# Performance work log

Hardware: AMD Instinct MI355X
Metric: run time of the kernel (lower is better)

## Reference

```python
import jax, jax.numpy as jnp
import numpy as np

V, L, D, DEMO, HID, N = 20000, 128, 256, 70, 1024, 2048


def setup_inputs() -> dict:
    key = jax.random.key(0)
    ks = jax.random.split(key, 16)
    s = 1.0 / np.sqrt(D)
    inp = {
        # learned parameters
        "E": jax.random.normal(ks[0], (V, D), jnp.float32) * 0.02,
        "Wq": jax.random.normal(ks[1], (D, D), jnp.float32) * s,
        "Wk": jax.random.normal(ks[2], (D, D), jnp.float32) * s,
        "Wv": jax.random.normal(ks[3], (D, D), jnp.float32) * s,
        "c_attn": jnp.ones((1,), jnp.float32) * 0.1,   # time_weight_net coefficient (attention decay)
        "c_pool": jnp.ones((1,), jnp.float32) * 0.5,   # history_repr Q_base-style pooling decay
        "W1": jax.random.normal(ks[4], (D + DEMO, HID), jnp.float32) * (1.0 / np.sqrt(D + DEMO)),
        "b1": jnp.zeros((HID,), jnp.float32),
        "W2": jax.random.normal(ks[5], (HID, 1), jnp.float32) * (1.0 / np.sqrt(HID)),
        "b2": jnp.zeros((1,), jnp.float32),
        # batched ragged task instances
        "demo": jax.random.normal(ks[6], (N, DEMO), jnp.float32),
        "hist_times": jax.random.uniform(ks[7], (N, L), jnp.float32) * 10.0,
        "event_time": jax.random.uniform(ks[8], (N,), jnp.float32) * 10.0 + 10.0,
        "labels": jax.random.randint(ks[9], (N,), 0, 2).astype(jnp.float32),
        "codes": jax.random.randint(ks[10], (N, L), 0, V),
        "lengths": jax.random.randint(ks[11], (N,), 1, L + 1).astype(jnp.int32),
    }
    return inp


def reference(E, Wq, Wk, Wv, c_attn, c_pool, W1, b1, W2, b2,
              demo, hist_times, event_time, labels, codes, lengths):
    POS_WEIGHT = 2.0
    NEG = jnp.float32(-1e9)
    mask = jnp.arange(L)[None, :] < lengths[:, None]            # [N, L] valid history positions

    emb = E[codes]                                              # [N, L, D] gather
    q = jnp.einsum('nld,de->nle', emb, Wq)
    k = jnp.einsum('nld,de->nle', emb, Wk)
    v = jnp.einsum('nld,de->nle', emb, Wv)

    # time-aware self-attention over each ragged history (masked)
    scores = jnp.einsum('nid,njd->nij', q, k) / jnp.sqrt(jnp.float32(D))
    dt = jnp.abs(hist_times[:, :, None] - hist_times[:, None, :])  # [N, L, L]
    scores = scores - c_attn[0] * dt
    scores = jnp.where(mask[:, None, :], scores, NEG)
    attn = jax.nn.softmax(scores, axis=-1)
    events = jnp.einsum('nij,njd->nid', attn, v)                # [N, L, D]

    # history_repr: time-decayed pooling toward event_time
    w = -c_pool[0] * (event_time[:, None] - hist_times)         # [N, L]
    w = jnp.where(mask, w, NEG)
    w = jax.nn.softmax(w, axis=-1)
    repr_ = jnp.einsum('nl,nld->nd', w, events)                 # [N, D]

    # disease/death classifier: demographics + history repr -> logit
    x = jnp.concatenate([demo, repr_], axis=-1)                 # [N, DEMO+D]
    h = jax.nn.relu(x @ W1 + b1)
    logit = (h @ W2 + b2)[:, 0]                                 # [N]

    # BCEWithLogitsLoss with pos_weight, averaged over valid predictions
    loss = -(POS_WEIGHT * labels * jax.nn.log_sigmoid(logit)
             + (1.0 - labels) * jax.nn.log_sigmoid(-logit))
    avg_loss = jnp.mean(loss)

    reg_loss = jnp.sum(c_attn ** 2) + jnp.sum(c_pool ** 2)      # time_weight_net.get_reg_loss()
    return avg_loss + reg_loss
```

## Files before the change

kernel.cpp:

```cpp
#include <hip/hip_runtime.h>
#include <hip/hip_bf16.h>
#include <math.h>
#include <stdint.h>

#define VV 20000
#define LL 128
#define DD 256
#define DEMO_ 70
#define HID_ 1024
#define NN 2048

typedef __attribute__((ext_vector_type(8))) short short8;
typedef __attribute__((ext_vector_type(4))) float f32x4;

__device__ __forceinline__ float bf2f(uint32_t u) {
    union { uint32_t u; float f; } c; c.u = u << 16; return c.f;
}
__device__ __forceinline__ uint32_t f2bf(float f) {
    union { float f; uint32_t u; } c; c.f = f;
    return (c.u + 0x7fffu + ((c.u >> 16) & 1u)) >> 16;
}

__device__ __forceinline__ int sw_off(int row, int col) {
    return (row << 8) + ((((col >> 3) ^ (row & 7)) << 3) | (col & 7));
}

__global__ __launch_bounds__(256) void k_init(const float* ca, const float* cp,
                                              float* z, float* out) {
    int idx = blockIdx.x * 256 + threadIdx.x;
    z[idx] = 0.f;
    if (idx == 0) out[0] = ca[0] * ca[0] + cp[0] * cp[0];
}

__global__ __launch_bounds__(256) void k_M(const float* __restrict__ Wq,
                                           const float* __restrict__ Wk,
                                           unsigned short* __restrict__ Mxf) {
    __shared__ float wq_s[DD];
    int e = blockIdx.x, t = threadIdx.x;
    wq_s[t] = Wq[(size_t)e * DD + t];
    __syncthreads();
    const float4* wk4 = (const float4*)(Wk + (size_t)t * DD);
    const float4* wq4 = (const float4*)wq_s;
    float4 acc = make_float4(0.f, 0.f, 0.f, 0.f);
    for (int c = 0; c < DD / 4; ++c) {
        float4 a = wq4[c]; float4 b = wk4[c];
        acc.x += a.x * b.x; acc.y += a.y * b.y;
        acc.z += a.z * b.z; acc.w += a.w * b.w;
    }
    float val = acc.x + acc.y + acc.z + acc.w;
    int frag = (e >> 4) * 8 + (t >> 5);
    int pos  = (((t >> 3) & 3) * 16 + (e & 15)) * 8 + (t & 7);
    Mxf[(size_t)frag * 512 + pos] = (unsigned short)f2bf(val);
}

__global__ __launch_bounds__(256) void k_prep(const float* __restrict__ Wv,
                                              const float* __restrict__ W1,
                                              unsigned short* __restrict__ W1f) {
    __shared__ float wv_s[DD];
    int k = blockIdx.x, t = threadIdx.x;
    int h = t + 256 * blockIdx.y;
    float val;
    if (k >= 326) {
        val = 0.f;
    } else if (k < DEMO_) {
        val = W1[(size_t)k * HID_ + h];
    } else {
        int e = k - DEMO_;
        wv_s[t] = Wv[(size_t)e * DD + t];
        __syncthreads();
        float acc = 0.f;
        for (int n = 0; n < DD; ++n)
            acc += wv_s[n] * W1[(size_t)(DEMO_ + n) * HID_ + h];
        val = acc;
    }
    int frag = (h >> 4) * 11 + (k >> 5);
    int pos  = (((k >> 3) & 3) * 16 + (h & 15)) * 8 + (k & 7);
    W1f[(size_t)frag * 512 + pos] = (unsigned short)f2bf(val);
}

__global__ __launch_bounds__(512, 4) void k_main(
    const float* __restrict__ E,
    const float* __restrict__ ht,  const float* __restrict__ evt_t,
    const int* __restrict__ codes, const int* __restrict__ lens,
    const float* __restrict__ ca_p, const float* __restrict__ cp_p,
    const unsigned short* __restrict__ Mxf,
    unsigned short* __restrict__ Rbf)
{
    __shared__ __align__(16) unsigned short emb_u[LL * DD];
    __shared__ float times_s[LL];
    __shared__ int   codes_s[LL];
    __shared__ float w_s[LL];
    __shared__ float apart[8][LL];
    __shared__ float rp_part[8][DD];
    __shared__ float asum[LL];

    const int n = blockIdx.x;
    const int tid = threadIdx.x, wv = tid >> 6, ln = tid & 63;
    const int q = ln >> 4, m = ln & 15;
    const int len = lens[n];
    const int it_n = (len + 15) >> 4;
    const float ca = ca_p[0], cp = cp_p[0];
    const float evt = evt_t[n];

    ((float*)apart)[tid]          = 0.f;
    ((float*)apart)[tid + 512]    = 0.f;
    ((float*)rp_part)[tid]        = 0.f;
    ((float*)rp_part)[tid + 512]  = 0.f;
    ((float*)rp_part)[tid + 1024] = 0.f;
    ((float*)rp_part)[tid + 1536] = 0.f;
    if (tid < LL) {
        w_s[tid] = 0.f;
        if (tid < len) {
            times_s[tid] = ht[(size_t)n * LL + tid];
            codes_s[tid] = codes[(size_t)n * LL + tid];
        }
    }
    __syncthreads();

    if (wv == 0) {
        float u0 = (ln      < len) ? cp * (times_s[ln]      - evt) : 0.f;
        float u1 = (ln + 64 < len) ? cp * (times_s[ln + 64] - evt) : 0.f;
        float e0 = (ln      < len) ? __expf(u0) : 0.f;
        float e1 = (ln + 64 < len) ? __expf(u1) : 0.f;
        float sm = e0 + e1;
        for (int o = 32; o; o >>= 1) sm += __shfl_xor(sm, o, 64);
        float inv = 1.f / sm;
        if (ln      < len) w_s[ln]      = e0 * inv;
        if (ln + 64 < len) w_s[ln + 64] = e1 * inv;
    }

    for (int l0 = wv; l0 < len; l0 += 32) {
        float4 v[4];
        #pragma unroll
        for (int u = 0; u < 4; ++u) {
            int l = l0 + u * 8;
            if (l < len)
                v[u] = ((const float4*)(E + (size_t)codes_s[l] * DD))[ln];
        }
        #pragma unroll
        for (int u = 0; u < 4; ++u) {
            int l = l0 + u * 8;
            if (l < len)
                *(uint2*)&emb_u[sw_off(l, 4 * ln)] =
                    make_uint2(f2bf(v[u].x) | (f2bf(v[u].y) << 16),
                               f2bf(v[u].z) | (f2bf(v[u].w) << 16));
        }
    }
    __syncthreads();

    short8 bB[2][8];
    #pragma unroll
    for (int nt = 0; nt < 2; ++nt)
        #pragma unroll
        for (int kk = 0; kk < 8; ++kk)
            bB[nt][kk] = *(const short8*)(Mxf + (size_t)((wv * 2 + nt) * 8 + kk) * 512 + ln * 8);

    short8 aC[8];
    for (int it = 0; it < it_n; ++it) {
        f32x4 h0 = (f32x4)0.f, h1 = (f32x4)0.f;
        #pragma unroll
        for (int kk = 0; kk < 8; ++kk) {
            short8 af = *(const short8*)&emb_u[sw_off(it * 16 + m, kk * 32 + q * 8)];
            if (it == wv) aC[kk] = af;
            h0 = __builtin_amdgcn_mfma_f32_16x16x32_bf16(af, bB[0][kk], h0, 0, 0, 0);
            h1 = __builtin_amdgcn_mfma_f32_16x16x32_bf16(af, bB[1][kk], h1, 0, 0, 0);
        }
        __syncthreads();
        #pragma unroll
        for (int r = 0; r < 4; ++r) {
            int row = it * 16 + q * 4 + r;
            emb_u[sw_off(row, wv * 32 + m)]      = (unsigned short)f2bf(h0[r]);
            emb_u[sw_off(row, wv * 32 + 16 + m)] = (unsigned short)f2bf(h1[r]);
        }
    }
    __syncthreads();

    if (wv < it_n) {
        f32x4 sac[8];
        #pragma unroll
        for (int jt = 0; jt < 8; ++jt) sac[jt] = (f32x4)0.f;
        for (int jt = 0; jt < it_n; ++jt) {
            #pragma unroll
            for (int kk = 0; kk < 8; ++kk) {
                short8 bH = *(const short8*)&emb_u[sw_off(jt * 16 + m, kk * 32 + q * 8)];
                sac[jt] = __builtin_amdgcn_mfma_f32_16x16x32_bf16(aC[kk], bH, sac[jt], 0, 0, 0);
            }
        }
        int i_base = wv * 16 + q * 4;
        float ti[4]; bool vR[4]; float rowsum[4];
        #pragma unroll
        for (int r = 0; r < 4; ++r) {
            vR[r] = (i_base + r) < len;
            ti[r] = times_s[i_base + r];
            rowsum[r] = 0.f;
        }
        for (int jt = 0; jt < it_n; ++jt) {
            int jcol = jt * 16 + m;
            bool vC = jcol < len;
            float tj = times_s[jcol];
            #pragma unroll
            for (int r = 0; r < 4; ++r) {
                float arg = sac[jt][r] * 0.0625f - ca * fabsf(ti[r] - tj);
                float p = (vR[r] && vC) ? __expf(arg) : 0.f;
                sac[jt][r] = p;
                rowsum[r] += p;
            }
        }
        #pragma unroll
        for (int r = 0; r < 4; ++r) {
            float s = rowsum[r];
            s += __shfl_xor(s, 1, 64); s += __shfl_xor(s, 2, 64);
            s += __shfl_xor(s, 4, 64); s += __shfl_xor(s, 8, 64);
            rowsum[r] = s;
        }
        float sc[4];
        #pragma unroll
        for (int r = 0; r < 4; ++r)
            sc[r] = (vR[r] && rowsum[r] > 0.f) ? w_s[i_base + r] / rowsum[r] : 0.f;
        for (int jt = 0; jt < it_n; ++jt) {
            float v = sc[0] * sac[jt][0] + sc[1] * sac[jt][1]
                    + sc[2] * sac[jt][2] + sc[3] * sac[jt][3];
            v += __shfl_xor(v, 16, 64);
            v += __shfl_xor(v, 32, 64);
            if (q == 0) apart[wv][jt * 16 + m] = v;
        }
    }
    __syncthreads();

    if (tid < LL)
        asum[tid] = apart[0][tid] + apart[1][tid] + apart[2][tid] + apart[3][tid]
                  + apart[4][tid] + apart[5][tid] + apart[6][tid] + apart[7][tid];
    __syncthreads();

    if (wv < it_n) {
        float aw = asum[wv * 16 + m];
        #pragma unroll
        for (int kk = 0; kk < 8; ++kk) {
            float v[8];
            #pragma unroll
            for (int j = 0; j < 8; ++j)
                v[j] = aw * bf2f((uint32_t)(unsigned short)aC[kk][j]);
            #pragma unroll
            for (int o = 1; o <= 8; o <<= 1)
                #pragma unroll
                for (int j = 0; j < 8; ++j)
                    v[j] += __shfl_xor(v[j], o, 64);
            if (m < 8)
                rp_part[wv][kk * 32 + q * 8 + m] = v[m];
        }
    }
    __syncthreads();
    if (tid < DD) {
        float r = rp_part[0][tid] + rp_part[1][tid] + rp_part[2][tid] + rp_part[3][tid]
                + rp_part[4][tid] + rp_part[5][tid] + rp_part[6][tid] + rp_part[7][tid];
        Rbf[(size_t)n * DD + tid] = (unsigned short)f2bf(r);
    }
}

__global__ __launch_bounds__(256) void k_mlp(
    const float* __restrict__ demo,
    const float* __restrict__ b1,   const float* __restrict__ W2,
    const unsigned short* __restrict__ Rbf,
    const unsigned short* __restrict__ W1f,
    float* __restrict__ z)
{
    __shared__ __align__(16) unsigned short xs[16][360];
    __shared__ float W2s[256];
    __shared__ float b1s[256];
    __shared__ float wred[4][16];

    const int tid = threadIdx.x, wv = tid >> 6, ln = tid & 63;
    const int q = ln >> 4, m = ln & 15;
    const int s0 = blockIdx.x * 16;
    const int by = blockIdx.y;
    const int hbase = by * 256;

    W2s[tid] = W2[hbase + tid];
    b1s[tid] = b1[hbase + tid];
    for (int s = 0; s < 16; ++s) {
        if (tid < DEMO_) xs[s][tid] = (unsigned short)f2bf(demo[(size_t)(s0 + s) * DEMO_ + tid]);
        xs[s][DEMO_ + tid] = Rbf[(size_t)(s0 + s) * DD + tid];
        if (tid < 34) xs[s][326 + tid] = 0;
    }
    __syncthreads();

    f32x4 cacc[4];
    #pragma unroll
    for (int ntl = 0; ntl < 4; ++ntl) cacc[ntl] = (f32x4)0.f;

    for (int kk = 0; kk < 11; ++kk) {
        short8 af = *(const short8*)&xs[m][kk * 32 + q * 8];
        #pragma unroll
        for (int ntl = 0; ntl < 4; ++ntl) {
            int frag = (by * 16 + wv * 4 + ntl) * 11 + kk;
            short8 bfd = *(const short8*)(W1f + (size_t)frag * 512 + ln * 8);
            cacc[ntl] = __builtin_amdgcn_mfma_f32_16x16x32_bf16(af, bfd, cacc[ntl], 0, 0, 0);
        }
    }

    float ls0 = 0.f, ls1 = 0.f, ls2 = 0.f, ls3 = 0.f;
    #pragma unroll
    for (int ntl = 0; ntl < 4; ++ntl) {
        int hl = wv * 64 + ntl * 16 + m;
        float bb = b1s[hl], w2v = W2s[hl];
        ls0 += fmaxf(cacc[ntl][0] + bb, 0.f) * w2v;
        ls1 += fmaxf(cacc[ntl][1] + bb, 0.f) * w2v;
        ls2 += fmaxf(cacc[ntl][2] + bb, 0.f) * w2v;
        ls3 += fmaxf(cacc[ntl][3] + bb, 0.f) * w2v;
    }
    #pragma unroll
    for (int o = 1; o <= 8; o <<= 1) {
        ls0 += __shfl_xor(ls0, o, 64); ls1 += __shfl_xor(ls1, o, 64);
        ls2 += __shfl_xor(ls2, o, 64); ls3 += __shfl_xor(ls3, o, 64);
    }
    if (m == 0) {
        wred[wv][q * 4 + 0] = ls0; wred[wv][q * 4 + 1] = ls1;
        wred[wv][q * 4 + 2] = ls2; wred[wv][q * 4 + 3] = ls3;
    }
    __syncthreads();
    if (tid < 16)
        atomicAdd(&z[s0 + tid], wred[0][tid] + wred[1][tid] + wred[2][tid] + wred[3][tid]);
}

__global__ __launch_bounds__(256) void k_loss(const float* __restrict__ labels,
                                              const float* __restrict__ b2,
                                              const float* __restrict__ z,
                                              float* __restrict__ out) {
    __shared__ float red[4];
    int tid = threadIdx.x, wv = tid >> 6;
    int i = blockIdx.x * 256 + tid;
    float zz = z[i] + b2[0];
    float y = labels[i];
    float lg = log1pf(__expf(-fabsf(zz)));
    float loss = 2.f * y * (fmaxf(-zz, 0.f) + lg) + (1.f - y) * (fmaxf(zz, 0.f) + lg);
    for (int o = 32; o; o >>= 1) loss += __shfl_xor(loss, o, 64);
    if ((tid & 63) == 0) red[wv] = loss;
    __syncthreads();
    if (tid == 0)
        atomicAdd(out, (red[0] + red[1] + red[2] + red[3]) * (1.f / (float)NN));
}

extern "C" void kernel_launch(void* const* d_in, const int* in_sizes, int n_in,
                              void* d_out, int out_size, void* d_ws, size_t ws_size,
                              hipStream_t stream) {
    const float* E      = (const float*)d_in[0];
    const float* Wq     = (const float*)d_in[1];
    const float* Wk     = (const float*)d_in[2];
    const float* Wv     = (const float*)d_in[3];
    const float* ca     = (const float*)d_in[4];
    const float* cp     = (const float*)d_in[5];
    const float* W1     = (const float*)d_in[6];
    const float* b1     = (const float*)d_in[7];
    const float* W2     = (const float*)d_in[8];
    const float* b2     = (const float*)d_in[9];
    const float* demo   = (const float*)d_in[10];
    const float* ht     = (const float*)d_in[11];
    const float* evt    = (const float*)d_in[12];
    const float* labels = (const float*)d_in[13];
    const int*   codes  = (const int*)d_in[14];
    const int*   lens   = (const int*)d_in[15];
    float* out = (float*)d_out;

    unsigned short* Mxf = (unsigned short*)d_ws;
    unsigned short* W1f = (unsigned short*)((char*)d_ws + 131072);
    unsigned short* Rbf = (unsigned short*)((char*)d_ws + 851968);
    float*          zar = (float*)((char*)d_ws + 1900544);

    hipLaunchKernelGGL(k_init, dim3(NN / 256), dim3(256), 0, stream, ca, cp, zar, out);
    hipLaunchKernelGGL(k_M,    dim3(DD), dim3(DD), 0, stream, Wq, Wk, Mxf);
    hipLaunchKernelGGL(k_prep, dim3(352, 4), dim3(256), 0, stream, Wv, W1, W1f);
    hipLaunchKernelGGL(k_main, dim3(NN), dim3(512), 0, stream,
                       E, ht, evt, codes, lens, ca, cp, Mxf, Rbf);
    hipLaunchKernelGGL(k_mlp,  dim3(NN / 16, 4), dim3(256), 0, stream,
                       demo, b1, W2, Rbf, W1f, zar);
    hipLaunchKernelGGL(k_loss, dim3(NN / 256), dim3(256), 0, stream, labels, b2, zar, out);
}
```

Measured before the change: 263.8 us.

## Merge prep kernels and schedule attention blocks longest-first by history length

Folds the init, Wq·Wk product and Wv·W1 prep kernels into one launch, which adds a block that counting-sorts instances by tile count so the main kernel processes longest histories first (LPT-style load balancing). The main kernel moves the Mxf fragment loads earlier to overlap with gathers and drops zero-initialisation of partial buffers. Reductions now sum only the active tiles. This cuts launch overhead and tail imbalance from ragged lengths, at the cost of an extra indirection and a serial sort block inside the prep launch.

```diff
diff --git a/kernel.cpp b/kernel.cpp
--- a/kernel.cpp
+++ b/kernel.cpp
@@ -25,57 +25,75 @@
     return (row << 8) + ((((col >> 3) ^ (row & 7)) << 3) | (col & 7));
 }
 
-__global__ __launch_bounds__(256) void k_init(const float* ca, const float* cp,
-                                              float* z, float* out) {
-    int idx = blockIdx.x * 256 + threadIdx.x;
-    z[idx] = 0.f;
-    if (idx == 0) out[0] = ca[0] * ca[0] + cp[0] * cp[0];
-}
-
-__global__ __launch_bounds__(256) void k_M(const float* __restrict__ Wq,
-                                           const float* __restrict__ Wk,
-                                           unsigned short* __restrict__ Mxf) {
-    __shared__ float wq_s[DD];
-    int e = blockIdx.x, t = threadIdx.x;
-    wq_s[t] = Wq[(size_t)e * DD + t];
-    __syncthreads();
-    const float4* wk4 = (const float4*)(Wk + (size_t)t * DD);
-    const float4* wq4 = (const float4*)wq_s;
-    float4 acc = make_float4(0.f, 0.f, 0.f, 0.f);
-    for (int c = 0; c < DD / 4; ++c) {
-        float4 a = wq4[c]; float4 b = wk4[c];
-        acc.x += a.x * b.x; acc.y += a.y * b.y;
-        acc.z += a.z * b.z; acc.w += a.w * b.w;
-    }
-    float val = acc.x + acc.y + acc.z + acc.w;
-    int frag = (e >> 4) * 8 + (t >> 5);
-    int pos  = (((t >> 3) & 3) * 16 + (e & 15)) * 8 + (t & 7);
-    Mxf[(size_t)frag * 512 + pos] = (unsigned short)f2bf(val);
-}
-
-__global__ __launch_bounds__(256) void k_prep(const float* __restrict__ Wv,
-                                              const float* __restrict__ W1,
-                                              unsigned short* __restrict__ W1f) {
-    __shared__ float wv_s[DD];
-    int k = blockIdx.x, t = threadIdx.x;
-    int h = t + 256 * blockIdx.y;
-    float val;
-    if (k >= 326) {
-        val = 0.f;
-    } else if (k < DEMO_) {
-        val = W1[(size_t)k * HID_ + h];
+__global__ __launch_bounds__(256) void k_pre(
+    const float* __restrict__ Wq, const float* __restrict__ Wk,
+    const float* __restrict__ Wv, const float* __restrict__ W1,
+    const float* __restrict__ ca, const float* __restrict__ cp,
+    const int* __restrict__ lens,
+    unsigned short* __restrict__ Mxf, unsigned short* __restrict__ W1f,
+    int* __restrict__ order, float* __restrict__ z, float* __restrict__ out)
+{
+    __shared__ float sm[DD];
+    __shared__ int cnt[9], off[9], cur[9];
+    const int b = blockIdx.x, t = threadIdx.x;
+
+    if (b < 256) {
+        int e = b;
+        sm[t] = Wq[(size_t)e * DD + t];
+        __syncthreads();
+        const float4* wk4 = (const float4*)(Wk + (size_t)t * DD);
+        const float4* wq4 = (const float4*)sm;
+        float4 acc = make_float4(0.f, 0.f, 0.f, 0.f);
+        for (int c = 0; c < DD / 4; ++c) {
+            float4 a = wq4[c]; float4 bb = wk4[c];
+            acc.x += a.x * bb.x; acc.y += a.y * bb.y;
+            acc.z += a.z * bb.z; acc.w += a.w * bb.w;
+        }
+        float val = acc.x + acc.y + acc.z + acc.w;
+        int frag = (e >> 4) * 8 + (t >> 5);
+        int pos  = (((t >> 3) & 3) * 16 + (e & 15)) * 8 + (t & 7);
+        Mxf[(size_t)frag * 512 + pos] = (unsigned short)f2bf(val);
+    } else if (b < 256 + 1408) {
+        int idx = b - 256;
+        int k = idx % 352, by = idx / 352;
+        int h = t + 256 * by;
+        float val;
+        if (k >= 326) {
+            val = 0.f;
+        } else if (k < DEMO_) {
+            val = W1[(size_t)k * HID_ + h];
+        } else {
+            int e = k - DEMO_;
+            sm[t] = Wv[(size_t)e * DD + t];
+            __syncthreads();
+            float acc = 0.f;
+            for (int n = 0; n < DD; ++n)
+                acc += sm[n] * W1[(size_t)(DEMO_ + n) * HID_ + h];
+            val = acc;
+        }
+        int frag = (h >> 4) * 11 + (k >> 5);
+        int pos  = (((k >> 3) & 3) * 16 + (h & 15)) * 8 + (k & 7);
+        W1f[(size_t)frag * 512 + pos] = (unsigned short)f2bf(val);
+    } else if (b == 1664) {
+        if (t < 9) cnt[t] = 0;
+        __syncthreads();
+        for (int i = t; i < NN; i += 256)
+            atomicAdd(&cnt[(lens[i] + 15) >> 4], 1);
+        __syncthreads();
+        if (t == 0) {
+            int acc = 0;
+            for (int k = 8; k >= 1; --k) { off[k] = acc; acc += cnt[k]; cur[k] = off[k]; }
+        }
+        __syncthreads();
+        for (int i = t; i < NN; i += 256) {
+            int key = (lens[i] + 15) >> 4;
+            int pos = atomicAdd(&cur[key], 1);
+            order[pos] = i;
+        }
     } else {
-        int e = k - DEMO_;
-        wv_s[t] = Wv[(size_t)e * DD + t];
-        __syncthreads();
-        float acc = 0.f;
-        for (int n = 0; n < DD; ++n)
-            acc += wv_s[n] * W1[(size_t)(DEMO_ + n) * HID_ + h];
-        val = acc;
-    }
-    int frag = (h >> 4) * 11 + (k >> 5);
-    int pos  = (((k >> 3) & 3) * 16 + (h & 15)) * 8 + (k & 7);
-    W1f[(size_t)frag * 512 + pos] = (unsigned short)f2bf(val);
+        for (int i = t; i < NN; i += 256) z[i] = 0.f;
+        if (t == 0) out[0] = ca[0] * ca[0] + cp[0] * cp[0];
+    }
 }
 
 __global__ __launch_bounds__(512, 4) void k_main(
@@ -84,6 +102,7 @@
     const int* __restrict__ codes, const int* __restrict__ lens,
     const float* __restrict__ ca_p, const float* __restrict__ cp_p,
     const unsigned short* __restrict__ Mxf,
+    const int* __restrict__ order,
     unsigned short* __restrict__ Rbf)
 {
     __shared__ __align__(16) unsigned short emb_u[LL * DD];
@@ -94,7 +113,7 @@
     __shared__ float rp_part[8][DD];
     __shared__ float asum[LL];
 
-    const int n = blockIdx.x;
+    const int n = order[blockIdx.x];
     const int tid = threadIdx.x, wv = tid >> 6, ln = tid & 63;
     const int q = ln >> 4, m = ln & 15;
     const int len = lens[n];
@@ -102,32 +121,30 @@
     const float ca = ca_p[0], cp = cp_p[0];
     const float evt = evt_t[n];
 
-    ((float*)apart)[tid]          = 0.f;
-    ((float*)apart)[tid + 512]    = 0.f;
-    ((float*)rp_part)[tid]        = 0.f;
-    ((float*)rp_part)[tid + 512]  = 0.f;
-    ((float*)rp_part)[tid + 1024] = 0.f;
-    ((float*)rp_part)[tid + 1536] = 0.f;
+    short8 bB[2][8];
+    #pragma unroll
+    for (int nt = 0; nt < 2; ++nt)
+        #pragma unroll
+        for (int kk = 0; kk < 8; ++kk)
+            bB[nt][kk] = *(const short8*)(Mxf + (size_t)((wv * 2 + nt) * 8 + kk) * 512 + ln * 8);
+
     if (tid < LL) {
-        w_s[tid] = 0.f;
-        if (tid < len) {
-            times_s[tid] = ht[(size_t)n * LL + tid];
-            codes_s[tid] = codes[(size_t)n * LL + tid];
-        }
-    }
-    __syncthreads();
-
+        bool v = tid < len;
+        times_s[tid] = v ? ht[(size_t)n * LL + tid] : 0.f;
+        codes_s[tid] = v ? codes[(size_t)n * LL + tid] : 0;
+    }
     if (wv == 0) {
-        float u0 = (ln      < len) ? cp * (times_s[ln]      - evt) : 0.f;
-        float u1 = (ln + 64 < len) ? cp * (times_s[ln + 64] - evt) : 0.f;
-        float e0 = (ln      < len) ? __expf(u0) : 0.f;
-        float e1 = (ln + 64 < len) ? __expf(u1) : 0.f;
-        float sm = e0 + e1;
-        for (int o = 32; o; o >>= 1) sm += __shfl_xor(sm, o, 64);
-        float inv = 1.f / sm;
+        float t0 = (ln      < len) ? ht[(size_t)n * LL + ln]      : 0.f;
+        float t1 = (ln + 64 < len) ? ht[(size_t)n * LL + ln + 64] : 0.f;
+        float e0 = (ln      < len) ? __expf(cp * (t0 - evt)) : 0.f;
+        float e1 = (ln + 64 < len) ? __expf(cp * (t1 - evt)) : 0.f;
+        float smm = e0 + e1;
+        for (int o = 32; o; o >>= 1) smm += __shfl_xor(smm, o, 64);
+        float inv = 1.f / smm;
         if (ln      < len) w_s[ln]      = e0 * inv;
         if (ln + 64 < len) w_s[ln + 64] = e1 * inv;
     }
+    __syncthreads();
 
     for (int l0 = wv; l0 < len; l0 += 32) {
         float4 v[4];
@@ -147,13 +164,6 @@
         }
     }
     __syncthreads();
-
-    short8 bB[2][8];
-    #pragma unroll
-    for (int nt = 0; nt < 2; ++nt)
-        #pragma unroll
-        for (int kk = 0; kk < 8; ++kk)
-            bB[nt][kk] = *(const short8*)(Mxf + (size_t)((wv * 2 + nt) * 8 + kk) * 512 + ln * 8);
 
     short8 aC[8];
     for (int it = 0; it < it_n; ++it) {
@@ -227,9 +237,11 @@
     }
     __syncthreads();
 
-    if (tid < LL)
-        asum[tid] = apart[0][tid] + apart[1][tid] + apart[2][tid] + apart[3][tid]
-                  + apart[4][tid] + apart[5][tid] + apart[6][tid] + apart[7][tid];
+    if (tid < LL) {
+        float s = 0.f;
+        for (int r = 0; r < it_n; ++r) s += apart[r][tid];
+        asum[tid] = s;
+    }
     __syncthreads();
 
     if (wv < it_n) {
@@ -251,8 +263,8 @@
     }
     __syncthreads();
     if (tid < DD) {
-        float r = rp_part[0][tid] + rp_part[1][tid] + rp_part[2][tid] + rp_part[3][tid]
-                + rp_part[4][tid] + rp_part[5][tid] + rp_part[6][tid] + rp_part[7][tid];
+        float r = 0.f;
+        for (int t = 0; t < it_n; ++t) r += rp_part[t][tid];
         Rbf[(size_t)n * DD + tid] = (unsigned short)f2bf(r);
     }
 }
@@ -365,12 +377,12 @@
     unsigned short* W1f = (unsigned short*)((char*)d_ws + 131072);
     unsigned short* Rbf = (unsigned short*)((char*)d_ws + 851968);
     float*          zar = (float*)((char*)d_ws + 1900544);
-
-    hipLaunchKernelGGL(k_init, dim3(NN / 256), dim3(256), 0, stream, ca, cp, zar, out);
-    hipLaunchKernelGGL(k_M,    dim3(DD), dim3(DD), 0, stream, Wq, Wk, Mxf);
-    hipLaunchKernelGGL(k_prep, dim3(352, 4), dim3(256), 0, stream, Wv, W1, W1f);
+    int*            ord = (int*)((char*)d_ws + 1908736);
+
+    hipLaunchKernelGGL(k_pre,  dim3(1666), dim3(256), 0, stream,
+                       Wq, Wk, Wv, W1, ca, cp, lens, Mxf, W1f, ord, zar, out);
     hipLaunchKernelGGL(k_main, dim3(NN), dim3(512), 0, stream,
-                       E, ht, evt, codes, lens, ca, cp, Mxf, Rbf);
+                       E, ht, evt, codes, lens, ca, cp, Mxf, ord, Rbf);
     hipLaunchKernelGGL(k_mlp,  dim3(NN / 16, 4), dim3(256), 0, stream,
                        demo, b1, W2, Rbf, W1f, zar);
     hipLaunchKernelGGL(k_loss, dim3(NN / 256), dim3(256), 0, stream, labels, b2, zar, out);
```

Result: faster. 227.8 us (-13.6%).
